# Optimization experiments

Hardware: AMD Instinct MI355X
Metric: run time of the kernel (lower is better)

## Reference

```python
import jax, jax.numpy as jnp
import numpy as np

B, T = 2, 512
D, H, DFF = 1024, 16, 4096
V, CSL = 32000, 16
NL, NDL = 4, 2
MAXLEN = 1024
DH = D // H


def generate_ar_mask(L, csl):
    m = np.zeros((2 * L, 2 * L), dtype=bool)
    for i in range(L):
        m[:i] = True
        m[L + (i // csl) * csl: L + i] = True
    return jnp.asarray(m)


def generate_block_ntp_mask(L, csl):
    m = np.zeros((2 * L, 2 * L), dtype=bool)
    for c in range(L // csl):
        if c - 1 >= 0:
            m[:(c - 1) * csl] = True
        m[L + c * csl: L + (c + 1) * csl] = True
    return jnp.asarray(m)


def layernorm(x, g, b, eps=1e-5):
    mu = x.mean(-1, keepdims=True)
    var = x.var(-1, keepdims=True)
    return (x - mu) / jnp.sqrt(var + eps) * g + b


def block(x, mask, p):
    ln1g, ln1b, wqkv, bqkv, wo, bo, ln2g, ln2b, w1, b1, w2, b2 = p
    h = layernorm(x, ln1g, ln1b)
    qkv = h @ wqkv + bqkv                       # [B,S,3D]
    q, k, v = jnp.split(qkv, 3, axis=-1)
    bs, S, _ = x.shape
    q = q.reshape(bs, S, H, DH).transpose(0, 2, 1, 3)
    k = k.reshape(bs, S, H, DH).transpose(0, 2, 1, 3)
    v = v.reshape(bs, S, H, DH).transpose(0, 2, 1, 3)
    scores = jnp.einsum('bhqd,bhkd->bhqk', q, k) / jnp.sqrt(jnp.asarray(DH, x.dtype))
    scores = jnp.where(mask, scores, jnp.asarray(-1e9, x.dtype))
    attn = jax.nn.softmax(scores, axis=-1)
    o = jnp.einsum('bhqk,bhkd->bhqd', attn, v)
    o = o.transpose(0, 2, 1, 3).reshape(bs, S, D)
    x = x + (o @ wo + bo)
    h = layernorm(x, ln2g, ln2b)
    return x + (jax.nn.gelu(h @ w1 + b1, approximate=False) @ w2 + b2)


def setup_inputs():
    key = jax.random.key(0)
    ks = jax.random.split(key, 6)

    def pstack(k, n):
        kk = jax.random.split(k, 4)
        return dict(
            ln1g=jnp.ones((n, D)), ln1b=jnp.zeros((n, D)),
            wqkv=0.02 * jax.random.normal(kk[0], (n, D, 3 * D)), bqkv=jnp.zeros((n, 3 * D)),
            wo=0.02 * jax.random.normal(kk[1], (n, D, D)), bo=jnp.zeros((n, D)),
            ln2g=jnp.ones((n, D)), ln2b=jnp.zeros((n, D)),
            w1=0.02 * jax.random.normal(kk[2], (n, D, DFF)), b1=jnp.zeros((n, DFF)),
            w2=0.02 * jax.random.normal(kk[3], (n, DFF, D)), b2=jnp.zeros((n, D)))

    body = pstack(ks[0], NL)
    dec = pstack(ks[1], NDL)
    inp = {
        'tok_ids': jax.random.randint(ks[2], (B, T), 0, V),
        'tok_emb': 0.02 * jax.random.normal(ks[3], (V, D)),
        'pos_emb': 0.02 * jax.random.normal(ks[4], (MAXLEN, D)),
        'mask_tokens': 0.02 * jax.random.normal(ks[5], (1, CSL, D)),
    }
    for kname, vv in body.items():
        inp['b_' + kname] = vv
    for kname, vv in dec.items():
        inp['d_' + kname] = vv
    return inp


def reference(tok_ids, tok_emb, pos_emb, mask_tokens,
              b_ln1g, b_ln1b, b_wqkv, b_bqkv, b_wo, b_bo, b_ln2g, b_ln2b, b_w1, b_b1, b_w2, b_b2,
              d_ln1g, d_ln1b, d_wqkv, d_bqkv, d_wo, d_bo, d_ln2g, d_ln2b, d_w1, d_b1, d_w2, d_b2):
    Bq, Tq = tok_ids.shape
    pos = jnp.tile(jnp.arange(Tq), 2)            # pos ids repeated for both halves
    emb_pos = pos_emb[pos]                       # [2T, D], broadcast over batch
    mask_ids = jnp.tile(mask_tokens, (Bq, Tq // CSL, 1))
    x = jnp.concatenate([tok_emb[tok_ids], mask_ids], axis=1) + emb_pos[None]

    body_mask = generate_block_ntp_mask(Tq, CSL)
    bp = (b_ln1g, b_ln1b, b_wqkv, b_bqkv, b_wo, b_bo, b_ln2g, b_ln2b, b_w1, b_b1, b_w2, b_b2)
    for i in range(NL):
        x = block(x, body_mask, tuple(p[i] for p in bp))

    ar_mask = generate_ar_mask(Tq, CSL)
    dp = (d_ln1g, d_ln1b, d_wqkv, d_bqkv, d_wo, d_bo, d_ln2g, d_ln2b, d_w1, d_b1, d_w2, d_b2)
    for i in range(NDL):
        x = block(x, ar_mask, tuple(p[i] for p in dp))

    logits = (x @ tok_emb.T)[:, Tq + 1:, :]      # [B, T-1, V]
    tgt = tok_ids[:, :-1].reshape(-1)
    logits = logits.reshape(-1, V)
    logp = jax.nn.log_softmax(logits, axis=-1)
    loss = -jnp.take_along_axis(logp, tgt[:, None], axis=1).mean()
    return loss
```

## Files before the change

### kernel.cpp

```cpp
#include <hip/hip_runtime.h>
#include <hip/hip_bf16.h>
#include <math.h>

#define DD   1024
#define HHN  16
#define DHD  64
#define DFFN 4096
#define VV   32000
#define BBN  2
#define TTN  512
#define SSN  1024
#define NRN  2048

typedef __attribute__((ext_vector_type(8))) short short8;
typedef __attribute__((ext_vector_type(4))) float f32x4;

enum : long {
    LSTR    = 12582912,
    OFF_QKV = 0,
    OFF_WO  = 3145728,
    OFF_W1  = 4194304,
    OFF_W2  = 8388608
};

struct P24 { const float* p[24]; };

__device__ __forceinline__ unsigned short f2bf(float f) {
    __hip_bfloat16 h = __float2bfloat16(f);
    return __builtin_bit_cast(unsigned short, h);
}
__device__ __forceinline__ float bf2f(unsigned short u) {
    return __bfloat162float(__builtin_bit_cast(__hip_bfloat16, u));
}

__device__ __forceinline__ void glds16(const void* g, void* l) {
    __builtin_amdgcn_global_load_lds(
        (const __attribute__((address_space(1))) void*)g,
        (__attribute__((address_space(3))) void*)l,
        16, 0, 0);
}

__device__ __forceinline__ float blockReduceSum(float v) {
    __shared__ float sh[4];
    #pragma unroll
    for (int o = 1; o < 64; o <<= 1) v += __shfl_xor(v, o, 64);
    int lane = threadIdx.x & 63, wv = threadIdx.x >> 6;
    __syncthreads();
    if (lane == 0) sh[wv] = v;
    __syncthreads();
    return sh[0] + sh[1] + sh[2] + sh[3];
}

__global__ __launch_bounds__(256) void prep_k(P24 wp, unsigned short* __restrict__ wbf,
                                              const int* __restrict__ tok,
                                              const float* __restrict__ temb,
                                              const float* __restrict__ pemb,
                                              const float* __restrict__ mtok,
                                              float* __restrict__ x) {
    __shared__ __align__(16) unsigned short Lb[128 * 72];
    const int id = blockIdx.x;
    const int t = threadIdx.x;

    if (id < 9216) {
        int seg, base, K, N;
        long woff;
        if (id < 2304)      { seg = 0; base = 0;    K = DD;   N = 3 * DD; woff = OFF_QKV; }
        else if (id < 3072) { seg = 1; base = 2304; K = DD;   N = DD;     woff = OFF_WO;  }
        else if (id < 6144) { seg = 2; base = 3072; K = DD;   N = DFFN;   woff = OFF_W1;  }
        else                { seg = 3; base = 6144; K = DFFN; N = DD;     woff = OFF_W2;  }
        const int rid = id - base;
        const int tpl = (K / 128) * (N / 64);
        const int lz = rid / tpl, t2 = rid % tpl;
        const int nt = N / 64;
        const int n0 = (t2 % nt) * 64, k0 = (t2 / nt) * 128;
        const float* w = wp.p[seg * 6 + lz];
        unsigned short* wt = wbf + (size_t)lz * LSTR + woff;

        const int kr = t >> 4;
        const int nc = (t & 15) * 4;
        #pragma unroll
        for (int p = 0; p < 8; p++) {
            const int k = p * 16 + kr;
            const int g = ((k >> 6) & 1) << 4;
            float4 f = *(const float4*)(w + (size_t)(k0 + k) * N + n0 + nc);
            __align__(8) unsigned short tmp[4];
            tmp[0] = f2bf(f.x); tmp[1] = f2bf(f.y);
            tmp[2] = f2bf(f.z); tmp[3] = f2bf(f.w);
            *(unsigned long long*)&Lb[k * 72 + (nc ^ g)] =
                *(const unsigned long long*)tmp;
        }
        __syncthreads();
        {
            const int rp  = t >> 3;
            const int sub = t & 7;
            const int kcg = sub >> 2;
            const int kh  = sub & 3;
            const int colx = (2 * rp) ^ (kcg << 4);
            const int kb = kcg * 64 + kh * 16;
            __align__(16) unsigned short tA[16], tB[16];
            #pragma unroll
            for (int i = 0; i < 16; i++) {
                unsigned int v = *(const unsigned int*)&Lb[(kb + i) * 72 + colx];
                tA[i] = (unsigned short)(v & 0xffff);
                tB[i] = (unsigned short)(v >> 16);
            }
            unsigned short* d0 = wt + (size_t)(n0 + 2 * rp) * K + k0 + kb;
            unsigned short* d1 = d0 + K;
            #pragma unroll
            for (int i = 0; i < 2; i++) {
                ((int4*)d0)[i] = ((const int4*)tA)[i];
                ((int4*)d1)[i] = ((const int4*)tB)[i];
            }
        }
    } else {
        const int row = id - 9216;
        const int b = row >> 10, s = row & 1023;
        const int d = t * 4;
        const float* src;
        const float* pe;
        if (s < TTN) {
            int tid2 = tok[b * TTN + s];
            src = temb + (size_t)tid2 * DD + d;
            pe  = pemb + (size_t)s * DD + d;
        } else {
            int sm = s - TTN;
            src = mtok + (size_t)(sm & 15) * DD + d;
            pe  = pemb + (size_t)sm * DD + d;
        }
        float4 v = *(const float4*)src;
        float4 p = *(const float4*)pe;
        v.x += p.x; v.y += p.y; v.z += p.z; v.w += p.w;
        *(float4*)(x + (size_t)row * DD + d) = v;
    }
}

__global__ __launch_bounds__(256) void ln_k(const float* __restrict__ x,
                                            const float* __restrict__ g,
                                            const float* __restrict__ b,
                                            unsigned short* __restrict__ out) {
    int row = blockIdx.x;
    int d = threadIdx.x * 4;
    const float4 v = *(const float4*)(x + (size_t)row * DD + d);
    float s  = v.x + v.y + v.z + v.w;
    float ss = v.x * v.x + v.y * v.y + v.z * v.z + v.w * v.w;
    s  = blockReduceSum(s);
    ss = blockReduceSum(ss);
    float mu  = s * (1.0f / DD);
    float var = ss * (1.0f / DD) - mu * mu;
    float inv = rsqrtf(var + 1e-5f);
    const float4 gg = *(const float4*)(g + d);
    const float4 bb = *(const float4*)(b + d);
    ushort4 o;
    o.x = f2bf((v.x - mu) * inv * gg.x + bb.x);
    o.y = f2bf((v.y - mu) * inv * gg.y + bb.y);
    o.z = f2bf((v.z - mu) * inv * gg.z + bb.z);
    o.w = f2bf((v.w - mu) * inv * gg.w + bb.w);
    *(ushort4*)(out + (size_t)row * DD + d) = o;
}

__global__ __launch_bounds__(256, 4) void flash_k(
    const unsigned short* __restrict__ qkvb,
    unsigned short* __restrict__ o,
    int mtype) {
    __shared__ __align__(16) unsigned short Qs[64][72];
    __shared__ __align__(16) unsigned short Ks[64][72];
    __shared__ __align__(16) unsigned short Vs[64][72];
    __shared__ __align__(16) unsigned short Ps[64][72];
    __shared__ float vcol[64];

    const int blk = blockIdx.x;
    const int bh = blk >> 4, qt = blk & 15;
    const int b = bh >> 4, h = bh & 15;
    const int t = threadIdx.x;
    const int lane = t & 63;
    const int w = t >> 6;
    const int fr = lane & 15;
    const int g8 = (lane >> 4) * 8;
    const int g4 = (lane >> 4) * 4;

    {
        const int r = t >> 2, c0 = (t & 3) * 16;
        const unsigned short* src =
            qkvb + (size_t)(b * SSN + qt * 64 + r) * 3072 + h * 64 + c0;
        *(int4*)&Qs[r][c0]     = *(const int4*)(src);
        *(int4*)&Qs[r][c0 + 8] = *(const int4*)(src + 8);
    }
    __syncthreads();
    short8 aq[2];
    #pragma unroll
    for (int kk = 0; kk < 2; kk++)
        aq[kk] = *(const short8*)&Qs[w * 16 + fr][kk * 32 + g8];

    float rsum[4] = {0.f, 0.f, 0.f, 0.f};
    f32x4 accO[4] = {};

    float vacc[16];
    #pragma unroll
    for (int j = 0; j < 16; j++) vacc[j] = 0.f;

    const unsigned short* kbase = qkvb + (size_t)(b * SSN) * 3072 + DD + h * 64;
    const unsigned short* vbase = qkvb + (size_t)(b * SSN) * 3072 + 2 * DD + h * 64;
    const int d0 = w * 16;

    for (int kt = 0; kt < 16; kt++) {
        __syncthreads();
        {
            const int r = t >> 2, c0 = (t & 3) * 16;
            const unsigned short* src = kbase + (size_t)(kt * 64 + r) * 3072 + c0;
            *(int4*)&Ks[r][c0]     = *(const int4*)(src);
            *(int4*)&Ks[r][c0 + 8] = *(const int4*)(src + 8);
        }
        {
            const unsigned short* src = vbase + (size_t)(kt * 64 + lane) * 3072 + d0;
            int4 q0 = *(const int4*)(src);
            int4 q1 = *(const int4*)(src + 8);
            const unsigned short* u = (const unsigned short*)&q0;
            #pragma unroll
            for (int j = 0; j < 8; j++) {
                Vs[d0 + j][lane] = u[j];
                vacc[j] += bf2f(u[j]);
            }
            const unsigned short* u2 = (const unsigned short*)&q1;
            #pragma unroll
            for (int j = 0; j < 8; j++) {
                Vs[d0 + 8 + j][lane] = u2[j];
                vacc[8 + j] += bf2f(u2[j]);
            }
        }
        __syncthreads();

        f32x4 a2[4] = {};
        #pragma unroll
        for (int n = 0; n < 4; n++) {
            short8 bk0 = *(const short8*)&Ks[n * 16 + fr][g8];
            short8 bk1 = *(const short8*)&Ks[n * 16 + fr][32 + g8];
            a2[n] = __builtin_amdgcn_mfma_f32_16x16x32_bf16(aq[0], bk0, a2[n], 0, 0, 0);
            a2[n] = __builtin_amdgcn_mfma_f32_16x16x32_bf16(aq[1], bk1, a2[n], 0, 0, 0);
        }
        #pragma unroll
        for (int j = 0; j < 4; j++) {
            #pragma unroll
            for (int n = 0; n < 4; n++) {
                float pv = __expf(a2[n][j] * 0.125f);
                rsum[j] += pv;
                Ps[w * 16 + g4 + j][n * 16 + fr] = f2bf(pv);
            }
        }
        #pragma unroll
        for (int kk = 0; kk < 2; kk++) {
            short8 pa = *(const short8*)&Ps[w * 16 + fr][kk * 32 + g8];
            #pragma unroll
            for (int nd = 0; nd < 4; nd++) {
                short8 vb = *(const short8*)&Vs[nd * 16 + fr][kk * 32 + g8];
                accO[nd] = __builtin_amdgcn_mfma_f32_16x16x32_bf16(pa, vb, accO[nd], 0, 0, 0);
            }
        }
    }

    float lrun[4];
    #pragma unroll
    for (int j = 0; j < 4; j++) {
        float rs = rsum[j];
        #pragma unroll
        for (int o2 = 1; o2 < 16; o2 <<= 1) rs += __shfl_xor(rs, o2, 64);
        lrun[j] = rs;
    }

    #pragma unroll
    for (int j = 0; j < 16; j++) {
        float vs = vacc[j];
        #pragma unroll
        for (int o2 = 1; o2 < 64; o2 <<= 1) vs += __shfl_xor(vs, o2, 64);
        if (lane == j) vcol[d0 + j] = vs;
    }
    __syncthreads();

    #pragma unroll
    for (int nd = 0; nd < 4; nd++)
        #pragma unroll
        for (int j = 0; j < 4; j++) {
            const int row = qt * 64 + w * 16 + g4 + j;
            const int col = nd * 16 + fr;
            bool uni;
            if (mtype == 0) uni = (row >= 480 && row < 512);
            else            uni = (row == 511) || (row >= 512 && (row & 15) == 15);
            float val;
            if (uni) val = vcol[col] * (1.0f / 1024.0f);
            else     val = accO[nd][j] / lrun[j];
            o[(size_t)(b * SSN + row) * DD + h * 64 + col] = f2bf(val);
        }
}

__global__ __launch_bounds__(256) void gxlconv_k(const float* __restrict__ x,
                                                 unsigned short* __restrict__ xl,
                                                 const float* __restrict__ temb,
                                                 unsigned short* __restrict__ tembb) {
    const int id = blockIdx.x;
    const int t = threadIdx.x;
    if (id < 1024) {
        int d = t * 4;
        ushort4 o = {0, 0, 0, 0};
        if (id < 1022) {
            int b = id / 511, i = id % 511;
            float4 v = *(const float4*)(x + (size_t)(b * SSN + 513 + i) * DD + d);
            o.x = f2bf(v.x); o.y = f2bf(v.y); o.z = f2bf(v.z); o.w = f2bf(v.w);
        }
        *(ushort4*)(xl + (size_t)id * DD + d) = o;
    } else {
        long i = ((long)(id - 1024) * 256 + t) * 8;
        float4 a = *(const float4*)(temb + i);
        float4 b = *(const float4*)(temb + i + 4);
        __align__(16) unsigned short tmp[8];
        tmp[0] = f2bf(a.x); tmp[1] = f2bf(a.y); tmp[2] = f2bf(a.z); tmp[3] = f2bf(a.w);
        tmp[4] = f2bf(b.x); tmp[5] = f2bf(b.y); tmp[6] = f2bf(b.z); tmp[7] = f2bf(b.w);
        *(int4*)(tembb + i) = *(const int4*)tmp;
    }
}

__global__ __launch_bounds__(256) void loss_row2_k(const float2* __restrict__ part,
                                                   const float* __restrict__ tgtlog,
                                                   float* __restrict__ rowloss) {
    const int r = blockIdx.x;
    const int t = threadIdx.x;
    float mx = -1e30f, s = 0.f;
    for (int i = t; i < 500; i += 256) {
        float2 p = part[(size_t)r * 500 + i];
        float m2 = fmaxf(mx, p.x);
        s = s * __expf(mx - m2) + p.y * __expf(p.x - m2);
        mx = m2;
    }
    #pragma unroll
    for (int o2 = 1; o2 < 64; o2 <<= 1) {
        float om = __shfl_xor(mx, o2, 64);
        float os = __shfl_xor(s, o2, 64);
        float m2 = fmaxf(mx, om);
        s = s * __expf(mx - m2) + os * __expf(om - m2);
        mx = m2;
    }
    __shared__ float shm[4], shs[4];
    int lane = t & 63, wv = t >> 6;
    if (lane == 0) { shm[wv] = mx; shs[wv] = s; }
    __syncthreads();
    if (t == 0) {
        float M = fmaxf(fmaxf(shm[0], shm[1]), fmaxf(shm[2], shm[3]));
        float S = shs[0] * __expf(shm[0] - M) + shs[1] * __expf(shm[1] - M)
                + shs[2] * __expf(shm[2] - M) + shs[3] * __expf(shm[3] - M);
        rowloss[r] = (logf(S) + M) - tgtlog[r];
    }
}

__global__ __launch_bounds__(256) void loss_final_k(const float* __restrict__ rowloss,
                                                    float* __restrict__ out) {
    int t = threadIdx.x;
    float s = 0.f;
    for (int i = t; i < 1022; i += 256) s += rowloss[i];
    s = blockReduceSum(s);
    if (t == 0) out[0] = s * (1.0f / 1022.0f);
}

template <int EPI, int KSPLIT, int BM>
__global__ __launch_bounds__(256) void gemm_k(
    const unsigned short* __restrict__ A, long lda,
    const unsigned short* __restrict__ Bt, long ldb,
    void* __restrict__ Cp, long ldc,
    const float* __restrict__ bias,
    int MT, int K, long kstr) {
    constexpr int MFRAG = BM / 32;
    __shared__ __align__(16) unsigned short As[2][BM][32];
    __shared__ __align__(16) unsigned short Bs[2][128][32];

    const int nwg = gridDim.x;
    const int q = nwg >> 3, r = nwg & 7;
    const int xcd = blockIdx.x & 7, lin = blockIdx.x >> 3;
    const int wg = (xcd < r ? xcd * (q + 1) : r * (q + 1) + (xcd - r) * q) + lin;
    const int tiles = nwg / KSPLIT;
    const int ks = wg / tiles;
    const int rem = wg % tiles;
    const int brow = (rem % MT) * BM;
    const int bcol = (rem / MT) * 128;
    const int Kl = K / KSPLIT;

    const int t = threadIdx.x;
    const int lane = t & 63;
    const int w = t >> 6;
    const int fr = lane & 15;
    const int g8 = (lane >> 4) * 8;

    const int sc = (lane & 3) * 8;
    const int srB = w * 32 + (lane >> 2);
    const unsigned short* bP0 = Bt + (size_t)(bcol + srB) * ldb + ks * Kl + sc;
    const unsigned short* bP1 = bP0 + (size_t)16 * ldb;
    const int srA = (BM == 128 ? w * 32 : w * 16) + (lane >> 2);
    const unsigned short* aP0 = A + (size_t)(brow + srA) * lda + ks * Kl + sc;
    const unsigned short* aP1 = aP0 + (size_t)16 * lda;

    f32x4 acc[MFRAG][4] = {};
    const int nsteps = Kl >> 5;

    auto stage = [&](int buf) {
        if constexpr (BM == 128) {
            glds16(aP0, &As[buf][w * 32][0]);
            glds16(aP1, &As[buf][w * 32 + 16][0]);
        } else {
            glds16(aP0, &As[buf][w * 16][0]);
        }
        glds16(bP0, &Bs[buf][w * 32][0]);
        glds16(bP1, &Bs[buf][w * 32 + 16][0]);
        aP0 += 32; aP1 += 32; bP0 += 32; bP1 += 32;
    };

    stage(0);
    asm volatile("s_waitcnt vmcnt(0)");
    __syncthreads();

    const int wrB = (w >> 1) * (BM / 2);
    int cur = 0;
    for (int s2 = 1; s2 < nsteps; ++s2) {
        const int nb = cur ^ 1;
        stage(nb);

        short8 af[MFRAG], bf[4];
        #pragma unroll
        for (int m = 0; m < MFRAG; m++)
            af[m] = *(const short8*)&As[cur][wrB + m * 16 + fr][g8];
        #pragma unroll
        for (int n = 0; n < 4; n++)
            bf[n] = *(const short8*)&Bs[cur][(w & 1) * 64 + n * 16 + fr][g8];
        #pragma unroll
        for (int m = 0; m < MFRAG; m++)
            #pragma unroll
            for (int n = 0; n < 4; n++)
                acc[m][n] = __builtin_amdgcn_mfma_f32_16x16x32_bf16(af[m], bf[n], acc[m][n], 0, 0, 0);
        __syncthreads();
        cur = nb;
    }
    {
        short8 af[MFRAG], bf[4];
        #pragma unroll
        for (int m = 0; m < MFRAG; m++)
            af[m] = *(const short8*)&As[cur][wrB + m * 16 + fr][g8];
        #pragma unroll
        for (int n = 0; n < 4; n++)
            bf[n] = *(const short8*)&Bs[cur][(w & 1) * 64 + n * 16 + fr][g8];
        #pragma unroll
        for (int m = 0; m < MFRAG; m++)
            #pragma unroll
            for (int n = 0; n < 4; n++)
                acc[m][n] = __builtin_amdgcn_mfma_f32_16x16x32_bf16(af[m], bf[n], acc[m][n], 0, 0, 0);
    }

    const int wc = (w & 1) * 64;
    const int g4 = (lane >> 4) * 4;
    #pragma unroll
    for (int n = 0; n < 4; n++) {
        const int col = bcol + wc + n * 16 + fr;
        const float bv = (bias && (KSPLIT == 1 || ks == 0)) ? bias[col] : 0.f;
        #pragma unroll
        for (int m = 0; m < MFRAG; m++) {
            #pragma unroll
            for (int j = 0; j < 4; j++) {
                const int row = brow + wrB + m * 16 + g4 + j;
                float v = acc[m][n][j] + bv;
                const size_t ci = (size_t)row * ldc + col;
                if (EPI == 0) {
                    ((float*)Cp)[ci] = v;
                } else if (EPI == 1) {
                    ((unsigned short*)Cp)[ci] = f2bf(v);
                } else if (EPI == 2) {
                    float gl = 0.5f * v * (1.0f + erff(v * 0.70710678118654752f));
                    ((unsigned short*)Cp)[ci] = f2bf(gl);
                } else if (EPI == 3) {
                    ((float*)Cp)[ci] += v;
                } else {
                    atomicAdd(&((float*)Cp)[ci], v);
                }
            }
        }
    }
}

__global__ __launch_bounds__(256) void gemm_lse_k(
    const unsigned short* __restrict__ A,
    const unsigned short* __restrict__ Bt,
    float2* __restrict__ part,
    float* __restrict__ tgtlog,
    const int* __restrict__ tok) {
    __shared__ __align__(16) unsigned short As[2][128][32];
    __shared__ __align__(16) unsigned short Bs[2][128][32];

    const int nwg = gridDim.x;
    const int q = nwg >> 3, r = nwg & 7;
    const int xcd = blockIdx.x & 7, lin = blockIdx.x >> 3;
    const int wg = (xcd < r ? xcd * (q + 1) : r * (q + 1) + (xcd - r) * q) + lin;
    const int MT = 8;
    const int brow = (wg % MT) * 128;
    const int bcol = (wg / MT) * 128;

    const int t = threadIdx.x;
    const int lane = t & 63;
    const int w = t >> 6;
    const int fr = lane & 15;
    const int g8 = (lane >> 4) * 8;

    const int sr = w * 32 + (lane >> 2);
    const int sc = (lane & 3) * 8;
    const unsigned short* aP0 = A + (size_t)(brow + sr) * DD + sc;
    const unsigned short* aP1 = aP0 + (size_t)16 * DD;
    const unsigned short* bP0 = Bt + (size_t)(bcol + sr) * DD + sc;
    const unsigned short* bP1 = bP0 + (size_t)16 * DD;

    f32x4 acc[4][4] = {};

    glds16(aP0, &As[0][w * 32][0]);
    glds16(aP1, &As[0][w * 32 + 16][0]);
    glds16(bP0, &Bs[0][w * 32][0]);
    glds16(bP1, &Bs[0][w * 32 + 16][0]);
    aP0 += 32; aP1 += 32; bP0 += 32; bP1 += 32;
    asm volatile("s_waitcnt vmcnt(0)");
    __syncthreads();

    int cur = 0;
    for (int s2 = 1; s2 < 32; ++s2) {
        const int nb = cur ^ 1;
        glds16(aP0, &As[nb][w * 32][0]);
        glds16(aP1, &As[nb][w * 32 + 16][0]);
        glds16(bP0, &Bs[nb][w * 32][0]);
        glds16(bP1, &Bs[nb][w * 32 + 16][0]);
        aP0 += 32; aP1 += 32; bP0 += 32; bP1 += 32;

        short8 af[4], bf[4];
        #pragma unroll
        for (int m = 0; m < 4; m++)
            af[m] = *(const short8*)&As[cur][(w >> 1) * 64 + m * 16 + fr][g8];
        #pragma unroll
        for (int n = 0; n < 4; n++)
            bf[n] = *(const short8*)&Bs[cur][(w & 1) * 64 + n * 16 + fr][g8];
        #pragma unroll
        for (int m = 0; m < 4; m++)
            #pragma unroll
            for (int n = 0; n < 4; n++)
                acc[m][n] = __builtin_amdgcn_mfma_f32_16x16x32_bf16(af[m], bf[n], acc[m][n], 0, 0, 0);
        __syncthreads();
        cur = nb;
    }
    {
        short8 af[4], bf[4];
        #pragma unroll
        for (int m = 0; m < 4; m++)
            af[m] = *(const short8*)&As[cur][(w >> 1) * 64 + m * 16 + fr][g8];
        #pragma unroll
        for (int n = 0; n < 4; n++)
            bf[n] = *(const short8*)&Bs[cur][(w & 1) * 64 + n * 16 + fr][g8];
        #pragma unroll
        for (int m = 0; m < 4; m++)
            #pragma unroll
            for (int n = 0; n < 4; n++)
                acc[m][n] = __builtin_amdgcn_mfma_f32_16x16x32_bf16(af[m], bf[n], acc[m][n], 0, 0, 0);
    }

    const int wr = (w >> 1) * 64;
    const int wc = (w & 1) * 64;
    const int g4 = (lane >> 4) * 4;
    const int ct2 = (bcol >> 7) * 2 + (w & 1);
    #pragma unroll
    for (int m = 0; m < 4; m++) {
        #pragma unroll
        for (int j = 0; j < 4; j++) {
            const int grow = brow + wr + m * 16 + g4 + j;
            const float v0 = acc[m][0][j], v1 = acc[m][1][j];
            const float v2 = acc[m][2][j], v3 = acc[m][3][j];
            float mx = fmaxf(fmaxf(v0, v1), fmaxf(v2, v3));
            #pragma unroll
            for (int o2 = 1; o2 < 16; o2 <<= 1) mx = fmaxf(mx, __shfl_xor(mx, o2, 64));
            float s = __expf(v0 - mx) + __expf(v1 - mx) + __expf(v2 - mx) + __expf(v3 - mx);
            #pragma unroll
            for (int o2 = 1; o2 < 16; o2 <<= 1) s += __shfl_xor(s, o2, 64);
            if (fr == 0) {
                float2 p; p.x = mx; p.y = s;
                part[(size_t)grow * 500 + ct2] = p;
            }
            int tgtc = -1;
            if (grow < 511) tgtc = tok[grow];
            else if (grow >= 511 && grow < 1022) tgtc = tok[512 + grow - 511];
            const int cl = tgtc - (bcol + wc);
            if (tgtc >= 0 && cl >= 0 && cl < 64 && (cl & 15) == fr) {
                const float vv[4] = {v0, v1, v2, v3};
                tgtlog[grow] = vv[cl >> 4];
            }
        }
    }
}

extern "C" void kernel_launch(void* const* d_in, const int* in_sizes, int n_in,
                              void* d_out, int out_size, void* d_ws, size_t ws_size,
                              hipStream_t stream) {
    const int*   tok  = (const int*)d_in[0];
    const float* temb = (const float*)d_in[1];
    const float* pemb = (const float*)d_in[2];
    const float* mtok = (const float*)d_in[3];
    const float* W[24];
    for (int i = 0; i < 24; i++) W[i] = (const float*)d_in[4 + i];

    char* ws = (char*)d_ws;
    float*          x      = (float*)(ws + 0);
    unsigned short* xb     = (unsigned short*)(ws + 8388608);
    unsigned short* qkvb   = (unsigned short*)(ws + 12582912);
    unsigned short* o      = (unsigned short*)(ws + 25165824);
    unsigned short* g      = (unsigned short*)(ws + 29360128);
    unsigned short* wbf    = (unsigned short*)(ws + 79691776);
    unsigned short* tembb  = (unsigned short*)(ws + 79691776);
    float2*         part   = (float2*)(ws + 145227776);
    float*          tgtlog = (float*)(ws + 149327872);
    unsigned short* xl     = (unsigned short*)(ws + 230686720);
    float*          rowloss= (float*)(ws + 232783872);

    P24 wp;
    for (int l = 0; l < 6; l++) {
        const int grp = (l < 4) ? 0 : 1;
        const int li  = (l < 4) ? l : l - 4;
        const float* const* P = W + grp * 12;
        wp.p[0 + l]  = P[2]  + (size_t)li * DD * 3 * DD;
        wp.p[6 + l]  = P[4]  + (size_t)li * DD * DD;
        wp.p[12 + l] = P[8]  + (size_t)li * DD * DFFN;
        wp.p[18 + l] = P[10] + (size_t)li * DFFN * DD;
    }
    prep_k<<<9216 + 2048, 256, 0, stream>>>(wp, wbf, tok, temb, pemb, mtok, x);

    for (int l = 0; l < 6; l++) {
        const int grp = (l < 4) ? 0 : 1;
        const int li  = (l < 4) ? l : l - 4;
        const float* const* P = W + grp * 12;
        const float* ln1g = P[0] + (size_t)li * DD;
        const float* ln1b = P[1] + (size_t)li * DD;
        const float* bqkv = P[3] + (size_t)li * 3 * DD;
        const float* bo   = P[5] + (size_t)li * DD;
        const float* ln2g = P[6] + (size_t)li * DD;
        const float* ln2b = P[7] + (size_t)li * DD;
        const float* b1   = P[9] + (size_t)li * DFFN;
        const float* b2   = P[11] + (size_t)li * DD;
        unsigned short* wl = wbf + (size_t)l * LSTR;

        if (l == 0) ln_k<<<NRN, 256, 0, stream>>>(x, ln1g, ln1b, xb);
        gemm_k<1, 1, 64><<<32 * 24, 256, 0, stream>>>(xb, DD, wl + OFF_QKV, DD,
                                                      qkvb, 3 * DD, bqkv, 32, DD, 0);
        flash_k<<<512, 256, 0, stream>>>(qkvb, o, grp);
        gemm_k<3, 1, 64><<<32 * 8, 256, 0, stream>>>(o, DD, wl + OFF_WO, DD,
                                                     x, DD, bo, 32, DD, 0);

        ln_k<<<NRN, 256, 0, stream>>>(x, ln2g, ln2b, xb);
        gemm_k<2, 1, 128><<<16 * 32, 256, 0, stream>>>(xb, DD, wl + OFF_W1, DD,
                                                       g, DFFN, b1, 16, DD, 0);
        gemm_k<4, 4, 128><<<16 * 8 * 4, 256, 0, stream>>>(g, DFFN, wl + OFF_W2, DFFN,
                                                          x, DD, b2, 16, DFFN, 0);
        if (l < 5) {
            const int l2 = l + 1;
            const int grp2 = (l2 < 4) ? 0 : 1;
            const int li2  = (l2 < 4) ? l2 : l2 - 4;
            const float* const* P2 = W + grp2 * 12;
            ln_k<<<NRN, 256, 0, stream>>>(x, P2[0] + (size_t)li2 * DD,
                                          P2[1] + (size_t)li2 * DD, xb);
        } else {
            gxlconv_k<<<1024 + 16000, 256, 0, stream>>>(x, xl, temb, tembb);
        }
    }

    gemm_lse_k<<<2000, 256, 0, stream>>>(xl, tembb, part, tgtlog, tok);
    loss_row2_k<<<1022, 256, 0, stream>>>(part, tgtlog, rowloss);
    loss_final_k<<<1, 256, 0, stream>>>(rowloss, (float*)d_out);
}
```

Measured before the change: 1.404 ms.

## Widen logits GEMM tile to 128x256 and fold final loss reduction into atomics

```diff
diff --git a/kernel.cpp b/kernel.cpp
--- a/kernel.cpp
+++ b/kernel.cpp
@@ -319,15 +319,13 @@
 
 __global__ __launch_bounds__(256) void loss_row2_k(const float2* __restrict__ part,
                                                    const float* __restrict__ tgtlog,
-                                                   float* __restrict__ rowloss) {
+                                                   float* __restrict__ out) {
     const int r = blockIdx.x;
     const int t = threadIdx.x;
     float mx = -1e30f, s = 0.f;
-    for (int i = t; i < 500; i += 256) {
-        float2 p = part[(size_t)r * 500 + i];
-        float m2 = fmaxf(mx, p.x);
-        s = s * __expf(mx - m2) + p.y * __expf(p.x - m2);
-        mx = m2;
+    if (t < 250) {
+        float2 p = part[(size_t)r * 250 + t];
+        mx = p.x; s = p.y;
     }
     #pragma unroll
     for (int o2 = 1; o2 < 64; o2 <<= 1) {
@@ -345,17 +343,8 @@
         float M = fmaxf(fmaxf(shm[0], shm[1]), fmaxf(shm[2], shm[3]));
         float S = shs[0] * __expf(shm[0] - M) + shs[1] * __expf(shm[1] - M)
                 + shs[2] * __expf(shm[2] - M) + shs[3] * __expf(shm[3] - M);
-        rowloss[r] = (logf(S) + M) - tgtlog[r];
-    }
-}
-
-__global__ __launch_bounds__(256) void loss_final_k(const float* __restrict__ rowloss,
-                                                    float* __restrict__ out) {
-    int t = threadIdx.x;
-    float s = 0.f;
-    for (int i = t; i < 1022; i += 256) s += rowloss[i];
-    s = blockReduceSum(s);
-    if (t == 0) out[0] = s * (1.0f / 1022.0f);
+        atomicAdd(out, ((logf(S) + M) - tgtlog[r]) * (1.0f / 1022.0f));
+    }
 }
 
 template <int EPI, int KSPLIT, int BM>
@@ -479,14 +468,14 @@
     }
 }
 
-__global__ __launch_bounds__(256) void gemm_lse_k(
+__global__ __launch_bounds__(256, 1) void gemm_lse_k(
     const unsigned short* __restrict__ A,
     const unsigned short* __restrict__ Bt,
     float2* __restrict__ part,
     float* __restrict__ tgtlog,
     const int* __restrict__ tok) {
     __shared__ __align__(16) unsigned short As[2][128][32];
-    __shared__ __align__(16) unsigned short Bs[2][128][32];
+    __shared__ __align__(16) unsigned short Bs[2][256][32];
 
     const int nwg = gridDim.x;
     const int q = nwg >> 3, r = nwg & 7;
@@ -494,7 +483,7 @@
     const int wg = (xcd < r ? xcd * (q + 1) : r * (q + 1) + (xcd - r) * q) + lin;
     const int MT = 8;
     const int brow = (wg % MT) * 128;
-    const int bcol = (wg / MT) * 128;
+    const int bcol = (wg / MT) * 256;
 
     const int t = threadIdx.x;
     const int lane = t & 63;
@@ -502,89 +491,99 @@
     const int fr = lane & 15;
     const int g8 = (lane >> 4) * 8;
 
-    const int sr = w * 32 + (lane >> 2);
     const int sc = (lane & 3) * 8;
-    const unsigned short* aP0 = A + (size_t)(brow + sr) * DD + sc;
+    const int srA = w * 32 + (lane >> 2);
+    const unsigned short* aP0 = A + (size_t)(brow + srA) * DD + sc;
     const unsigned short* aP1 = aP0 + (size_t)16 * DD;
-    const unsigned short* bP0 = Bt + (size_t)(bcol + sr) * DD + sc;
+    const int srB = w * 64 + (lane >> 2);
+    const unsigned short* bP0 = Bt + (size_t)(bcol + srB) * DD + sc;
     const unsigned short* bP1 = bP0 + (size_t)16 * DD;
-
-    f32x4 acc[4][4] = {};
-
-    glds16(aP0, &As[0][w * 32][0]);
-    glds16(aP1, &As[0][w * 32 + 16][0]);
-    glds16(bP0, &Bs[0][w * 32][0]);
-    glds16(bP1, &Bs[0][w * 32 + 16][0]);
-    aP0 += 32; aP1 += 32; bP0 += 32; bP1 += 32;
+    const unsigned short* bP2 = bP0 + (size_t)32 * DD;
+    const unsigned short* bP3 = bP0 + (size_t)48 * DD;
+
+    f32x4 acc[4][8] = {};
+
+    auto stage = [&](int buf) {
+        glds16(aP0, &As[buf][w * 32][0]);
+        glds16(aP1, &As[buf][w * 32 + 16][0]);
+        glds16(bP0, &Bs[buf][w * 64][0]);
+        glds16(bP1, &Bs[buf][w * 64 + 16][0]);
+        glds16(bP2, &Bs[buf][w * 64 + 32][0]);
+        glds16(bP3, &Bs[buf][w * 64 + 48][0]);
+        aP0 += 32; aP1 += 32;
+        bP0 += 32; bP1 += 32; bP2 += 32; bP3 += 32;
+    };
+
+    stage(0);
     asm volatile("s_waitcnt vmcnt(0)");
     __syncthreads();
 
     int cur = 0;
     for (int s2 = 1; s2 < 32; ++s2) {
         const int nb = cur ^ 1;
-        glds16(aP0, &As[nb][w * 32][0]);
-        glds16(aP1, &As[nb][w * 32 + 16][0]);
-        glds16(bP0, &Bs[nb][w * 32][0]);
-        glds16(bP1, &Bs[nb][w * 32 + 16][0]);
-        aP0 += 32; aP1 += 32; bP0 += 32; bP1 += 32;
-
-        short8 af[4], bf[4];
+        stage(nb);
+
+        short8 af[4], bf[8];
         #pragma unroll
         for (int m = 0; m < 4; m++)
             af[m] = *(const short8*)&As[cur][(w >> 1) * 64 + m * 16 + fr][g8];
         #pragma unroll
-        for (int n = 0; n < 4; n++)
-            bf[n] = *(const short8*)&Bs[cur][(w & 1) * 64 + n * 16 + fr][g8];
+        for (int n = 0; n < 8; n++)
+            bf[n] = *(const short8*)&Bs[cur][(w & 1) * 128 + n * 16 + fr][g8];
         #pragma unroll
         for (int m = 0; m < 4; m++)
             #pragma unroll
-            for (int n = 0; n < 4; n++)
+            for (int n = 0; n < 8; n++)
                 acc[m][n] = __builtin_amdgcn_mfma_f32_16x16x32_bf16(af[m], bf[n], acc[m][n], 0, 0, 0);
         __syncthreads();
         cur = nb;
     }
     {
-        short8 af[4], bf[4];
+        short8 af[4], bf[8];
         #pragma unroll
         for (int m = 0; m < 4; m++)
             af[m] = *(const short8*)&As[cur][(w >> 1) * 64 + m * 16 + fr][g8];
         #pragma unroll
-        for (int n = 0; n < 4; n++)
-            bf[n] = *(const short8*)&Bs[cur][(w & 1) * 64 + n * 16 + fr][g8];
+        for (int n = 0; n < 8; n++)
+            bf[n] = *(const short8*)&Bs[cur][(w & 1) * 128 + n * 16 + fr][g8];
         #pragma unroll
         for (int m = 0; m < 4; m++)
             #pragma unroll
-            for (int n = 0; n < 4; n++)
+            for (int n = 0; n < 8; n++)
                 acc[m][n] = __builtin_amdgcn_mfma_f32_16x16x32_bf16(af[m], bf[n], acc[m][n], 0, 0, 0);
     }
 
     const int wr = (w >> 1) * 64;
-    const int wc = (w & 1) * 64;
+    const int wc = (w & 1) * 128;
     const int g4 = (lane >> 4) * 4;
-    const int ct2 = (bcol >> 7) * 2 + (w & 1);
+    const int ct2 = (bcol >> 7) + (w & 1);
     #pragma unroll
     for (int m = 0; m < 4; m++) {
         #pragma unroll
         for (int j = 0; j < 4; j++) {
             const int grow = brow + wr + m * 16 + g4 + j;
-            const float v0 = acc[m][0][j], v1 = acc[m][1][j];
-            const float v2 = acc[m][2][j], v3 = acc[m][3][j];
-            float mx = fmaxf(fmaxf(v0, v1), fmaxf(v2, v3));
+            float vv[8];
+            #pragma unroll
+            for (int n = 0; n < 8; n++) vv[n] = acc[m][n][j];
+            float mx = vv[0];
+            #pragma unroll
+            for (int n = 1; n < 8; n++) mx = fmaxf(mx, vv[n]);
             #pragma unroll
             for (int o2 = 1; o2 < 16; o2 <<= 1) mx = fmaxf(mx, __shfl_xor(mx, o2, 64));
-            float s = __expf(v0 - mx) + __expf(v1 - mx) + __expf(v2 - mx) + __expf(v3 - mx);
+            float s = 0.f;
+            #pragma unroll
+            for (int n = 0; n < 8; n++) s += __expf(vv[n] - mx);
             #pragma unroll
             for (int o2 = 1; o2 < 16; o2 <<= 1) s += __shfl_xor(s, o2, 64);
             if (fr == 0) {
                 float2 p; p.x = mx; p.y = s;
-                part[(size_t)grow * 500 + ct2] = p;
+                part[(size_t)grow * 250 + ct2] = p;
             }
             int tgtc = -1;
             if (grow < 511) tgtc = tok[grow];
             else if (grow >= 511 && grow < 1022) tgtc = tok[512 + grow - 511];
             const int cl = tgtc - (bcol + wc);
-            if (tgtc >= 0 && cl >= 0 && cl < 64 && (cl & 15) == fr) {
-                const float vv[4] = {v0, v1, v2, v3};
+            if (tgtc >= 0 && cl >= 0 && cl < 128 && (cl & 15) == fr) {
                 tgtlog[grow] = vv[cl >> 4];
             }
         }
@@ -610,9 +609,10 @@
     unsigned short* wbf    = (unsigned short*)(ws + 79691776);
     unsigned short* tembb  = (unsigned short*)(ws + 79691776);
     float2*         part   = (float2*)(ws + 145227776);
-    float*          tgtlog = (float*)(ws + 149327872);
+    float*          tgtlog = (float*)(ws + 147275776);
     unsigned short* xl     = (unsigned short*)(ws + 230686720);
     float*          rowloss= (float*)(ws + 232783872);
+    (void)rowloss;
 
     P24 wp;
     for (int l = 0; l < 6; l++) {
@@ -624,6 +624,7 @@
         wp.p[12 + l] = P[8]  + (size_t)li * DD * DFFN;
         wp.p[18 + l] = P[10] + (size_t)li * DFFN * DD;
     }
+    hipMemsetAsync(d_out, 0, 4, stream);
     prep_k<<<9216 + 2048, 256, 0, stream>>>(wp, wbf, tok, temb, pemb, mtok, x);
 
     for (int l = 0; l < 6; l++) {
@@ -664,7 +665,6 @@
         }
     }
 
-    gemm_lse_k<<<2000, 256, 0, stream>>>(xl, tembb, part, tgtlog, tok);
-    loss_row2_k<<<1022, 256, 0, stream>>>(part, tgtlog, rowloss);
-    loss_final_k<<<1, 256, 0, stream>>>(rowloss, (float*)d_out);
-}
+    gemm_lse_k<<<1000, 256, 0, stream>>>(xl, tembb, part, tgtlog, tok);
+    loss_row2_k<<<1022, 256, 0, stream>>>(part, tgtlog, (float*)d_out);
+}
```

New measurement: 1.414 ms. Within noise of the previous version (+0.8%).
